# Performance work log

Hardware: AMD Instinct MI355X
Metric: run time of the kernel (lower is better)

Reference implementation:

```python
import jax, jax.numpy as jnp
import numpy as np

S, A, B, D = 4, 64, 2048, 384
H1, H2, H3 = 128, 128, 64


def setup_inputs() -> dict:
    key = jax.random.key(0)
    ks = jax.random.split(key, 6)
    x = jax.random.normal(ks[0], (B, A, D), dtype=jnp.float32)
    species = jax.random.randint(ks[1], (A,), 0, S, dtype=jnp.int32)
    # per-species stacked MLP weights, scaled ~1/sqrt(fan_in) like reset_parameters
    W0 = jax.random.normal(ks[2], (S, D, H1), dtype=jnp.float32) / np.sqrt(D)
    W1 = jax.random.normal(ks[3], (S, H1, H2), dtype=jnp.float32) / np.sqrt(H1)
    W2 = jax.random.normal(ks[4], (S, H2, H3), dtype=jnp.float32) / np.sqrt(H2)
    W3 = jax.random.normal(ks[5], (S, H3, 1), dtype=jnp.float32) / np.sqrt(H3)
    b0 = jnp.zeros((S, H1), jnp.float32)
    b1 = jnp.zeros((S, H2), jnp.float32)
    b2 = jnp.zeros((S, H3), jnp.float32)
    b3 = jnp.zeros((S, 1), jnp.float32)
    return {"x": x, "species": species, "W0": W0, "b0": b0, "W1": W1,
            "b1": b1, "W2": W2, "b2": b2, "W3": W3, "b3": b3}


def reference(x, species, W0, b0, W1, b1, W2, b2, W3, b3):
    # Gather per-atom species weights once, then batched per-atom GEMMs.
    # x: [B, A, D]; species: [A]
    y = jnp.einsum('bad,adh->bah', x, W0[species]) + b0[species]
    y = jnp.exp(-y * y)
    y = jnp.einsum('bah,ahk->bak', y, W1[species]) + b1[species]
    y = jnp.exp(-y * y)
    y = jnp.einsum('bak,akm->bam', y, W2[species]) + b2[species]
    y = jnp.exp(-y * y)
    y = jnp.einsum('bam,amo->bao', y, W3[species]) + b3[species]  # [B, A, 1]
    return jnp.squeeze(jnp.sum(y, axis=1))  # [B]
```

## Files before the change

kernel.cpp:

```cpp
#include <hip/hip_runtime.h>

#define S_DIM 4
#define A_DIM 64
#define B_DIM 2048
#define D_DIM 384
#define H1D 128
#define H2D 128
#define H3D 64
#define MT 64
#define XROW (A_DIM * D_DIM)

typedef __attribute__((ext_vector_type(8))) short short8;
typedef __attribute__((ext_vector_type(4))) float float4v;

__device__ __forceinline__ unsigned short f2bf(float f) {
  unsigned u = __float_as_uint(f);
  u += 0x7FFFu + ((u >> 16) & 1u);
  return (unsigned short)(u >> 16);
}

__device__ __forceinline__ void store_bf4(unsigned short* p, float4v v) {
  union { unsigned short s[4]; uint2 u; } t;
  t.s[0] = f2bf(v[0]); t.s[1] = f2bf(v[1]);
  t.s[2] = f2bf(v[2]); t.s[3] = f2bf(v[3]);
  *(uint2*)p = t.u;
}

__global__ __launch_bounds__(256) void prep_weights(
    const float* __restrict__ W0, const float* __restrict__ W1,
    const float* __restrict__ W2,
    unsigned short* __restrict__ W0T, unsigned short* __restrict__ W1T,
    unsigned short* __restrict__ W2T) {
  __shared__ float tile[32][33];
  int b = blockIdx.x;
  const float* src; unsigned short* dst; int R, C, dt, ht, s;
  if (b < 192) {
    s = b / 48; int t = b % 48; dt = t / 4; ht = t % 4;
    src = W0 + s * D_DIM * H1D; dst = W0T + s * H1D * D_DIM; R = D_DIM; C = H1D;
  } else if (b < 256) {
    int bb = b - 192; s = bb / 16; int t = bb % 16; dt = t / 4; ht = t % 4;
    src = W1 + s * H1D * H2D; dst = W1T + s * H2D * H1D; R = H1D; C = H2D;
  } else {
    int bb = b - 256; s = bb / 8; int t = bb % 8; dt = t / 2; ht = t % 2;
    src = W2 + s * H2D * H3D; dst = W2T + s * H3D * H2D; R = H2D; C = H3D;
  }
  int tx = threadIdx.x & 31, ty = threadIdx.x >> 5;
#pragma unroll
  for (int k = 0; k < 4; ++k)
    tile[ty + 8 * k][tx] = src[(size_t)(dt * 32 + ty + 8 * k) * C + ht * 32 + tx];
  __syncthreads();
#pragma unroll
  for (int k = 0; k < 4; ++k)
    dst[(size_t)(ht * 32 + ty + 8 * k) * R + dt * 32 + tx] = f2bf(tile[tx][ty + 8 * k]);
}

__global__ __launch_bounds__(256, 4) void mlp_fused(
    const float* __restrict__ x, const int* __restrict__ species,
    const unsigned short* __restrict__ W0T, const unsigned short* __restrict__ W1T,
    const unsigned short* __restrict__ W2T,
    const float* __restrict__ b0, const float* __restrict__ b1,
    const float* __restrict__ b2, const float* __restrict__ W3,
    const float* __restrict__ b3, float* __restrict__ out) {
  __shared__ __align__(16) unsigned short xbuf0[MT * 136];
  __shared__ __align__(16) unsigned short xbuf1[MT * 136];
  __shared__ float W3s[H3D];
  unsigned short* H0 = xbuf1;
  unsigned short* H1 = xbuf0;
  float* H2 = (float*)xbuf1;

  const int a = blockIdx.x;
  const int brow0 = blockIdx.y * MT;
  const int sp = species[a];
  const int tid = threadIdx.x;
  const int wave = tid >> 6;
  const int lane = tid & 63;
  const int q = lane >> 4;
  const int r = lane & 15;

  const float4v zero = {0.f, 0.f, 0.f, 0.f};

  const int srow16 = tid >> 4;
  const int c16 = tid & 15;
  const float* xbase = x + ((size_t)(brow0 + srow16) * A_DIM + a) * D_DIM + c16 * 4;
  unsigned short* xd0 = xbuf0 + srow16 * 136 + c16 * 4;
  unsigned short* xd1 = xbuf1 + srow16 * 136 + c16 * 4;
  const unsigned short* w0base =
      W0T + (size_t)sp * H1D * D_DIM + (wave * 32 + r) * D_DIM + q * 8;

  float4v xv[8];
#pragma unroll
  for (int h = 0; h < 4; ++h) {
    xv[2 * h]     = *(const float4v*)(xbase + (size_t)h * 16 * XROW);
    xv[2 * h + 1] = *(const float4v*)(xbase + (size_t)h * 16 * XROW + 64);
  }
  if (tid < H3D) W3s[tid] = W3[sp * H3D + tid];
  short8 bf[4][2];
#pragma unroll
  for (int kk = 0; kk < 4; ++kk)
#pragma unroll
    for (int n = 0; n < 2; ++n)
      bf[kk][n] = *(const short8*)(w0base + n * 16 * D_DIM + kk * 32);
#pragma unroll
  for (int h = 0; h < 4; ++h) {
    store_bf4(xd0 + h * 16 * 136, xv[2 * h]);
    store_bf4(xd0 + h * 16 * 136 + 64, xv[2 * h + 1]);
  }
  __syncthreads();

  float4v acc0[4][2];
#pragma unroll
  for (int g = 0; g < 4; ++g) { acc0[g][0] = zero; acc0[g][1] = zero; }

#pragma unroll
  for (int h = 0; h < 4; ++h) {
    xv[2 * h]     = *(const float4v*)(xbase + (size_t)h * 16 * XROW + 128);
    xv[2 * h + 1] = *(const float4v*)(xbase + (size_t)h * 16 * XROW + 192);
  }
#pragma unroll
  for (int g = 0; g < 4; ++g)
#pragma unroll
    for (int kk = 0; kk < 4; ++kk) {
      short8 af = *(const short8*)(xbuf0 + (g * 16 + r) * 136 + kk * 32 + q * 8);
      acc0[g][0] = __builtin_amdgcn_mfma_f32_16x16x32_bf16(af, bf[kk][0], acc0[g][0], 0, 0, 0);
      acc0[g][1] = __builtin_amdgcn_mfma_f32_16x16x32_bf16(af, bf[kk][1], acc0[g][1], 0, 0, 0);
    }
#pragma unroll
  for (int h = 0; h < 4; ++h) {
    store_bf4(xd1 + h * 16 * 136, xv[2 * h]);
    store_bf4(xd1 + h * 16 * 136 + 64, xv[2 * h + 1]);
  }
  __syncthreads();

#pragma unroll
  for (int kk = 0; kk < 4; ++kk)
#pragma unroll
    for (int n = 0; n < 2; ++n)
      bf[kk][n] = *(const short8*)(w0base + n * 16 * D_DIM + 128 + kk * 32);
#pragma unroll
  for (int h = 0; h < 4; ++h) {
    xv[2 * h]     = *(const float4v*)(xbase + (size_t)h * 16 * XROW + 256);
    xv[2 * h + 1] = *(const float4v*)(xbase + (size_t)h * 16 * XROW + 320);
  }
#pragma unroll
  for (int g = 0; g < 4; ++g)
#pragma unroll
    for (int kk = 0; kk < 4; ++kk) {
      short8 af = *(const short8*)(xbuf1 + (g * 16 + r) * 136 + kk * 32 + q * 8);
      acc0[g][0] = __builtin_amdgcn_mfma_f32_16x16x32_bf16(af, bf[kk][0], acc0[g][0], 0, 0, 0);
      acc0[g][1] = __builtin_amdgcn_mfma_f32_16x16x32_bf16(af, bf[kk][1], acc0[g][1], 0, 0, 0);
    }
#pragma unroll
  for (int h = 0; h < 4; ++h) {
    store_bf4(xd0 + h * 16 * 136, xv[2 * h]);
    store_bf4(xd0 + h * 16 * 136 + 64, xv[2 * h + 1]);
  }
  __syncthreads();

#pragma unroll
  for (int kk = 0; kk < 4; ++kk)
#pragma unroll
    for (int n = 0; n < 2; ++n)
      bf[kk][n] = *(const short8*)(w0base + n * 16 * D_DIM + 256 + kk * 32);
#pragma unroll
  for (int g = 0; g < 4; ++g)
#pragma unroll
    for (int kk = 0; kk < 4; ++kk) {
      short8 af = *(const short8*)(xbuf0 + (g * 16 + r) * 136 + kk * 32 + q * 8);
      acc0[g][0] = __builtin_amdgcn_mfma_f32_16x16x32_bf16(af, bf[kk][0], acc0[g][0], 0, 0, 0);
      acc0[g][1] = __builtin_amdgcn_mfma_f32_16x16x32_bf16(af, bf[kk][1], acc0[g][1], 0, 0, 0);
    }
  {
    const float* b0p = b0 + sp * H1D;
#pragma unroll
    for (int n = 0; n < 2; ++n) {
      float bias = b0p[wave * 32 + n * 16 + r];
#pragma unroll
      for (int g = 0; g < 4; ++g)
#pragma unroll
        for (int i = 0; i < 4; ++i) {
          float y = acc0[g][n][i] + bias;
          H0[(g * 16 + q * 4 + i) * 136 + wave * 32 + n * 16 + r] = f2bf(__expf(-y * y));
        }
    }
  }
  __syncthreads();

  {
    float4v acc1[4][2];
#pragma unroll
    for (int g = 0; g < 4; ++g) { acc1[g][0] = zero; acc1[g][1] = zero; }
    const unsigned short* w1base =
        W1T + (size_t)sp * H2D * H1D + (wave * 32 + r) * H1D + q * 8;
    short8 wf[4][2];
#pragma unroll
    for (int kk = 0; kk < 4; ++kk)
#pragma unroll
      for (int n = 0; n < 2; ++n)
        wf[kk][n] = *(const short8*)(w1base + n * 16 * H1D + kk * 32);
#pragma unroll
    for (int g = 0; g < 4; ++g)
#pragma unroll
      for (int kk = 0; kk < 4; ++kk) {
        short8 af = *(const short8*)(H0 + (g * 16 + r) * 136 + kk * 32 + q * 8);
        acc1[g][0] = __builtin_amdgcn_mfma_f32_16x16x32_bf16(af, wf[kk][0], acc1[g][0], 0, 0, 0);
        acc1[g][1] = __builtin_amdgcn_mfma_f32_16x16x32_bf16(af, wf[kk][1], acc1[g][1], 0, 0, 0);
      }
    const float* b1p = b1 + sp * H2D;
#pragma unroll
    for (int n = 0; n < 2; ++n) {
      float bias = b1p[wave * 32 + n * 16 + r];
#pragma unroll
      for (int g = 0; g < 4; ++g)
#pragma unroll
        for (int i = 0; i < 4; ++i) {
          float y = acc1[g][n][i] + bias;
          H1[(g * 16 + q * 4 + i) * 136 + wave * 32 + n * 16 + r] = f2bf(__expf(-y * y));
        }
    }
  }
  __syncthreads();

  {
    float4v acc2[4];
#pragma unroll
    for (int g = 0; g < 4; ++g) acc2[g] = zero;
    const unsigned short* w2base =
        W2T + (size_t)sp * H3D * H2D + (wave * 16 + r) * H2D + q * 8;
    short8 wf[4];
#pragma unroll
    for (int kk = 0; kk < 4; ++kk)
      wf[kk] = *(const short8*)(w2base + kk * 32);
#pragma unroll
    for (int g = 0; g < 4; ++g)
#pragma unroll
      for (int kk = 0; kk < 4; ++kk) {
        short8 af = *(const short8*)(H1 + (g * 16 + r) * 136 + kk * 32 + q * 8);
        acc2[g] = __builtin_amdgcn_mfma_f32_16x16x32_bf16(af, wf[kk], acc2[g], 0, 0, 0);
      }
    float bias = b2[sp * H3D + wave * 16 + r];
#pragma unroll
    for (int g = 0; g < 4; ++g)
#pragma unroll
      for (int i = 0; i < 4; ++i) {
        float y = acc2[g][i] + bias;
        H2[(g * 16 + q * 4 + i) * 68 + wave * 16 + r] = __expf(-y * y);
      }
  }
  __syncthreads();

  {
    const int row = tid >> 2;
    const int seg = tid & 3;
    const float4v* h2p = (const float4v*)(H2 + row * 68 + seg * 16);
    const float4v* w3p = (const float4v*)(W3s + seg * 16);
    float4v sv = zero;
#pragma unroll
    for (int jj = 0; jj < 4; ++jj) sv += h2p[jj] * w3p[jj];
    float s = sv[0] + sv[1] + sv[2] + sv[3];
    s += __shfl_xor(s, 1);
    s += __shfl_xor(s, 2);
    if (seg == 0) atomicAdd(&out[brow0 + row], s + b3[sp]);
  }
}

extern "C" void kernel_launch(void* const* d_in, const int* in_sizes, int n_in,
                              void* d_out, int out_size, void* d_ws, size_t ws_size,
                              hipStream_t stream) {
  const float* x       = (const float*)d_in[0];
  const int*   species = (const int*)d_in[1];
  const float* W0 = (const float*)d_in[2];
  const float* b0 = (const float*)d_in[3];
  const float* W1 = (const float*)d_in[4];
  const float* b1 = (const float*)d_in[5];
  const float* W2 = (const float*)d_in[6];
  const float* b2 = (const float*)d_in[7];
  const float* W3 = (const float*)d_in[8];
  const float* b3 = (const float*)d_in[9];
  float* out = (float*)d_out;

  unsigned short* W0T = (unsigned short*)d_ws;
  unsigned short* W1T = W0T + S_DIM * H1D * D_DIM;
  unsigned short* W2T = W1T + S_DIM * H2D * H1D;

  hipMemsetAsync(d_out, 0, out_size * sizeof(float), stream);
  prep_weights<<<dim3(288), dim3(256), 0, stream>>>(W0, W1, W2, W0T, W1T, W2T);
  mlp_fused<<<dim3(A_DIM, B_DIM / MT), dim3(256), 0, stream>>>(
      x, species, W0T, W1T, W2T, b0, b1, b2, W3, b3, out);
}
```

Before: 305.5 us.

## Prefetch x chunks deeper, use LDS-only barriers, replace atomics with partial-sum reduction

```diff
diff --git a/kernel.cpp b/kernel.cpp
--- a/kernel.cpp
+++ b/kernel.cpp
@@ -25,6 +25,13 @@
   t.s[2] = f2bf(v[2]); t.s[3] = f2bf(v[3]);
   *(uint2*)p = t.u;
 }
+
+#define LGKM_BARRIER()                                        \
+  do {                                                        \
+    asm volatile("s_waitcnt lgkmcnt(0)" ::: "memory");        \
+    __builtin_amdgcn_s_barrier();                             \
+    asm volatile("" ::: "memory");                            \
+  } while (0)
 
 __global__ __launch_bounds__(256) void prep_weights(
     const float* __restrict__ W0, const float* __restrict__ W1,
@@ -54,13 +61,13 @@
     dst[(size_t)(ht * 32 + ty + 8 * k) * R + dt * 32 + tx] = f2bf(tile[tx][ty + 8 * k]);
 }
 
-__global__ __launch_bounds__(256, 4) void mlp_fused(
+__global__ __launch_bounds__(256, 3) void mlp_fused(
     const float* __restrict__ x, const int* __restrict__ species,
     const unsigned short* __restrict__ W0T, const unsigned short* __restrict__ W1T,
     const unsigned short* __restrict__ W2T,
     const float* __restrict__ b0, const float* __restrict__ b1,
     const float* __restrict__ b2, const float* __restrict__ W3,
-    const float* __restrict__ b3, float* __restrict__ out) {
+    const float* __restrict__ b3, float* __restrict__ partial) {
   __shared__ __align__(16) unsigned short xbuf0[MT * 136];
   __shared__ __align__(16) unsigned short xbuf1[MT * 136];
   __shared__ float W3s[H3D];
@@ -87,12 +94,17 @@
   const unsigned short* w0base =
       W0T + (size_t)sp * H1D * D_DIM + (wave * 32 + r) * D_DIM + q * 8;
 
-  float4v xv[8];
+  float4v xv[8], xw[8];
 #pragma unroll
   for (int h = 0; h < 4; ++h) {
     xv[2 * h]     = *(const float4v*)(xbase + (size_t)h * 16 * XROW);
     xv[2 * h + 1] = *(const float4v*)(xbase + (size_t)h * 16 * XROW + 64);
   }
+#pragma unroll
+  for (int h = 0; h < 4; ++h) {
+    xw[2 * h]     = *(const float4v*)(xbase + (size_t)h * 16 * XROW + 128);
+    xw[2 * h + 1] = *(const float4v*)(xbase + (size_t)h * 16 * XROW + 192);
+  }
   if (tid < H3D) W3s[tid] = W3[sp * H3D + tid];
   short8 bf[4][2];
 #pragma unroll
@@ -105,7 +117,7 @@
     store_bf4(xd0 + h * 16 * 136, xv[2 * h]);
     store_bf4(xd0 + h * 16 * 136 + 64, xv[2 * h + 1]);
   }
-  __syncthreads();
+  LGKM_BARRIER();
 
   float4v acc0[4][2];
 #pragma unroll
@@ -113,8 +125,13 @@
 
 #pragma unroll
   for (int h = 0; h < 4; ++h) {
-    xv[2 * h]     = *(const float4v*)(xbase + (size_t)h * 16 * XROW + 128);
-    xv[2 * h + 1] = *(const float4v*)(xbase + (size_t)h * 16 * XROW + 192);
+    store_bf4(xd1 + h * 16 * 136, xw[2 * h]);
+    store_bf4(xd1 + h * 16 * 136 + 64, xw[2 * h + 1]);
+  }
+#pragma unroll
+  for (int h = 0; h < 4; ++h) {
+    xw[2 * h]     = *(const float4v*)(xbase + (size_t)h * 16 * XROW + 256);
+    xw[2 * h + 1] = *(const float4v*)(xbase + (size_t)h * 16 * XROW + 320);
   }
 #pragma unroll
   for (int g = 0; g < 4; ++g)
@@ -124,23 +141,13 @@
       acc0[g][0] = __builtin_amdgcn_mfma_f32_16x16x32_bf16(af, bf[kk][0], acc0[g][0], 0, 0, 0);
       acc0[g][1] = __builtin_amdgcn_mfma_f32_16x16x32_bf16(af, bf[kk][1], acc0[g][1], 0, 0, 0);
     }
-#pragma unroll
-  for (int h = 0; h < 4; ++h) {
-    store_bf4(xd1 + h * 16 * 136, xv[2 * h]);
-    store_bf4(xd1 + h * 16 * 136 + 64, xv[2 * h + 1]);
-  }
-  __syncthreads();
+  LGKM_BARRIER();
 
 #pragma unroll
   for (int kk = 0; kk < 4; ++kk)
 #pragma unroll
     for (int n = 0; n < 2; ++n)
       bf[kk][n] = *(const short8*)(w0base + n * 16 * D_DIM + 128 + kk * 32);
-#pragma unroll
-  for (int h = 0; h < 4; ++h) {
-    xv[2 * h]     = *(const float4v*)(xbase + (size_t)h * 16 * XROW + 256);
-    xv[2 * h + 1] = *(const float4v*)(xbase + (size_t)h * 16 * XROW + 320);
-  }
 #pragma unroll
   for (int g = 0; g < 4; ++g)
 #pragma unroll
@@ -151,10 +158,10 @@
     }
 #pragma unroll
   for (int h = 0; h < 4; ++h) {
-    store_bf4(xd0 + h * 16 * 136, xv[2 * h]);
-    store_bf4(xd0 + h * 16 * 136 + 64, xv[2 * h + 1]);
-  }
-  __syncthreads();
+    store_bf4(xd0 + h * 16 * 136, xw[2 * h]);
+    store_bf4(xd0 + h * 16 * 136 + 64, xw[2 * h + 1]);
+  }
+  LGKM_BARRIER();
 
 #pragma unroll
   for (int kk = 0; kk < 4; ++kk)
@@ -259,8 +266,17 @@
     float s = sv[0] + sv[1] + sv[2] + sv[3];
     s += __shfl_xor(s, 1);
     s += __shfl_xor(s, 2);
-    if (seg == 0) atomicAdd(&out[brow0 + row], s + b3[sp]);
-  }
+    if (seg == 0) partial[(size_t)a * B_DIM + brow0 + row] = s + b3[sp];
+  }
+}
+
+__global__ __launch_bounds__(256) void reduce_partial(
+    const float* __restrict__ p, float* __restrict__ out) {
+  const int b = blockIdx.x * 256 + threadIdx.x;
+  float s = 0.f;
+#pragma unroll
+  for (int a = 0; a < A_DIM; ++a) s += p[(size_t)a * B_DIM + b];
+  out[b] = s;
 }
 
 extern "C" void kernel_launch(void* const* d_in, const int* in_sizes, int n_in,
@@ -281,9 +297,10 @@
   unsigned short* W0T = (unsigned short*)d_ws;
   unsigned short* W1T = W0T + S_DIM * H1D * D_DIM;
   unsigned short* W2T = W1T + S_DIM * H2D * H1D;
-
-  hipMemsetAsync(d_out, 0, out_size * sizeof(float), stream);
+  float* partial = (float*)(W2T + S_DIM * H3D * H2D);
+
   prep_weights<<<dim3(288), dim3(256), 0, stream>>>(W0, W1, W2, W0T, W1T, W2T);
   mlp_fused<<<dim3(A_DIM, B_DIM / MT), dim3(256), 0, stream>>>(
-      x, species, W0T, W1T, W2T, b0, b1, b2, W3, b3, out);
-}
+      x, species, W0T, W1T, W2T, b0, b1, b2, W3, b3, partial);
+  reduce_partial<<<dim3(B_DIM / 256), dim3(256), 0, stream>>>(partial, out);
+}
```

Result: slower. 324.6 us (+6.3%).
